# Kernel tuning notes

Hardware: AMD Instinct MI355X
Metric: run time of the kernel (lower is better)

Reference implementation:

```python
import jax, jax.numpy as jnp
import numpy as np

B, L, CIN, H, K = 32, 4096, 128, 256, 3


def setup_inputs() -> dict:
    key = jax.random.key(0)
    k1, k2, k3 = jax.random.split(key, 3)
    x = jax.random.normal(k1, (B, L, CIN), dtype=jnp.float32)
    # Conv1d weight: (out_ch=3H, in_ch=CIN, kernel=K), fan-in scaled like torch default
    W = jax.random.normal(k2, (3 * H, CIN, K), dtype=jnp.float32) * (1.0 / np.sqrt(CIN * K))
    b = jax.random.normal(k3, (3 * H,), dtype=jnp.float32) * 0.01
    return {"x": x, "W": W, "b": b}


def reference(x, W, b):
    # x: (B, L, CIN) -> (B, CIN, L), matching torch's x.transpose(1, 2)
    xc = jnp.transpose(x, (0, 2, 1))
    # valid 1D conv -> (B, 3H, T) with T = L - K + 1
    conv = jax.lax.conv_general_dilated(
        xc, W, window_strides=(1,), padding="VALID",
        dimension_numbers=("NCH", "OIH", "NCH"),
    ) + b[None, :, None]
    Z, F, O = jnp.split(conv, 3, axis=1)
    Z = jnp.tanh(Z)
    F = jax.nn.sigmoid(F)
    O = jax.nn.sigmoid(O)
    # sequential fo-pool: h_t = O_t * (F_t * h_{t-1} + (1 - F_t) * Z_t)
    zs = jnp.moveaxis(Z, 2, 0)   # (T, B, H)
    fs = jnp.moveaxis(F, 2, 0)
    os_ = jnp.moveaxis(O, 2, 0)
    h0 = jnp.zeros((x.shape[0], H), dtype=Z.dtype)

    def step(h, zfo):
        z, f, o = zfo
        h = o * (f * h + (1.0 - f) * z)
        return h, None

    hT, _ = jax.lax.scan(step, h0, (zs, fs, os_))
    return hT  # (B, H): final hidden state
```

## Files before the change

### kernel.cpp

```cpp
#include <hip/hip_runtime.h>
#include <math.h>

#define B_    32
#define L_    4096
#define CIN_  128
#define H_    256
#define T_    4094
#define KTOT_ 384

#define MT_   64
#define NTB_  64
#define NKT_  12

typedef float f32x4 __attribute__((ext_vector_type(4)));
typedef short s16x8 __attribute__((ext_vector_type(8)));

static __device__ __forceinline__ unsigned short f2bf(float f) {
  unsigned u = __builtin_bit_cast(unsigned, f);
  u = (u + 0x7FFFu + ((u >> 16) & 1u)) >> 16;
  return (unsigned short)u;
}

__global__ __launch_bounds__(256) void packW_bf16(const float* __restrict__ W,
                                                  unsigned short* __restrict__ Wb) {
  const int idx = blockIdx.x * 256 + threadIdx.x;
  const int c = idx % 768;
  const int t = idx / 768;
  const int kgrp = t & 3;
  const int kt = t >> 2;
  const int q = c >> 4, lr = c & 15;
  const int gate = q % 3, hgrp = q / 3;
  const int oc = gate * 256 + hgrp * 16 + lr;
  s16x8 outv;
#pragma unroll
  for (int e = 0; e < 8; ++e) {
    const int kk = kt * 32 + kgrp * 8 + e;
    const int i = kk & 127, k = kk >> 7;
    outv[e] = (short)f2bf(W[(size_t)oc * KTOT_ + i * 3 + k]);
  }
  *(s16x8*)(Wb + (size_t)idx * 8) = outv;
}

__global__ __launch_bounds__(1024, 4) void conv_scan_mfma(
    const float* __restrict__ x, const unsigned short* __restrict__ Wb,
    const float* __restrict__ bias, float* __restrict__ Pc,
    float* __restrict__ Sc) {
  __shared__ __align__(16) char xs[66 * 256];

  const int tid = threadIdx.x;
  const int wn = tid >> 6;
  const int l = tid & 63;
  const int lr = l & 15;
  const int lg = l >> 4;
  const int bid = blockIdx.x;
  const int bb = bid & 31;
  const int tblk = bid >> 5;
  const int t0 = tblk * MT_;

  const unsigned short* bp = Wb + lg * 6144 + (wn * 48 + lr) * 8;

  s16x8 bcur[3];
#pragma unroll
  for (int nj = 0; nj < 3; ++nj)
    bcur[nj] = *(const s16x8*)(bp + nj * 128);

  for (int v = tid; v < 66 * 32; v += 1024) {
    const int row = v >> 5;
    const int colb = (v & 31) * 8;
    int r = t0 + row;
    if (r > L_ - 1) r = L_ - 1;
    const float4 xv = *(const float4*)&x[((size_t)bb * L_ + r) * CIN_ + (v & 31) * 4];
    unsigned p0, p1;
    asm("v_cvt_pk_bf16_f32 %0, %1, %2" : "=v"(p0) : "v"(xv.x), "v"(xv.y));
    asm("v_cvt_pk_bf16_f32 %0, %1, %2" : "=v"(p1) : "v"(xv.z), "v"(xv.w));
    *(uint2*)(xs + row * 256 + (colb ^ ((row & 7) << 4))) = make_uint2(p0, p1);
  }

  f32x4 acc[4][3];
#pragma unroll
  for (int mi = 0; mi < 4; ++mi)
#pragma unroll
    for (int nj = 0; nj < 3; ++nj) acc[mi][nj] = (f32x4)0.f;

  __syncthreads();

#pragma unroll
  for (int kt = 0; kt < NKT_; ++kt) {
    s16x8 bnxt[3];
    if (kt < NKT_ - 1) {
#pragma unroll
      for (int nj = 0; nj < 3; ++nj)
        bnxt[nj] = *(const s16x8*)(bp + (kt + 1) * 24576 + nj * 128);
    }
    const int kof = kt >> 2;
    const int cb = (kt & 3) * 64 + lg * 16;
    s16x8 a[4];
#pragma unroll
    for (int mi = 0; mi < 4; ++mi) {
      const int row = mi * 16 + lr + kof;
      a[mi] = *(const s16x8*)(xs + row * 256 + (cb ^ ((row & 7) << 4)));
    }
#pragma unroll
    for (int mi = 0; mi < 4; ++mi)
#pragma unroll
      for (int nj = 0; nj < 3; ++nj)
        acc[mi][nj] = __builtin_amdgcn_mfma_f32_16x16x32_bf16(a[mi], bcur[nj], acc[mi][nj], 0, 0, 0);
    if (kt < NKT_ - 1) {
#pragma unroll
      for (int nj = 0; nj < 3; ++nj) bcur[nj] = bnxt[nj];
    }
  }

  const int hl = wn * 16 + lr;
  const float bz = bias[hl];
  const float bf_ = bias[256 + hl];
  const float bo_ = bias[512 + hl];

  float Pw = 1.f, Sw = 0.f;
#pragma unroll
  for (int mi = 0; mi < 4; ++mi) {
    float Pr = 1.f, Sr = 0.f;
#pragma unroll
    for (int r = 0; r < 4; ++r) {
      const int t = t0 + mi * 16 + lg * 4 + r;
      const float zr = acc[mi][0][r] + bz;
      const float fr = acc[mi][1][r] + bf_;
      const float orr = acc[mi][2][r] + bo_;
      const float zc = fminf(fmaxf(zr, -15.f), 15.f);
      const float e2 = __expf(2.f * zc);
      const float zt = (e2 - 1.f) * __builtin_amdgcn_rcpf(e2 + 1.f);
      const float ft = __builtin_amdgcn_rcpf(1.f + __expf(-fr));
      const float ot = __builtin_amdgcn_rcpf(1.f + __expf(-orr));
      float A = ot * ft;
      float Bv = ot * (1.f - ft) * zt;
      const bool valid = (t < T_);
      A = valid ? A : 1.f;
      Bv = valid ? Bv : 0.f;
      Sr = A * Sr + Bv;
      Pr = A * Pr;
    }
    float Pp = __shfl_xor(Pr, 16), Sp = __shfl_xor(Sr, 16);
    if (lg & 1) { Sr = Pr * Sp + Sr; Pr = Pr * Pp; }
    else        { Sr = Pp * Sr + Sp; Pr = Pp * Pr; }
    Pp = __shfl_xor(Pr, 32); Sp = __shfl_xor(Sr, 32);
    if (lg & 2) { Sr = Pr * Sp + Sr; Pr = Pr * Pp; }
    else        { Sr = Pp * Sr + Sp; Pr = Pp * Pr; }
    Sw = Pr * Sw + Sr;
    Pw = Pr * Pw;
  }

  if (lg == 0) {
    const size_t o = ((size_t)bb * NTB_ + tblk) * H_ + hl;
    Pc[o] = Pw;
    Sc[o] = Sw;
  }
}

__global__ __launch_bounds__(128) void combine_kernel(const float* __restrict__ Pc,
                                                      const float* __restrict__ Sc,
                                                      float* __restrict__ out) {
  const int idx = blockIdx.x * 128 + threadIdx.x;
  const int b = idx >> 8;
  const int h = idx & 255;
  float hv = 0.f;
#pragma unroll 8
  for (int c = 0; c < NTB_; ++c) {
    const float p = Pc[((size_t)b * NTB_ + c) * H_ + h];
    const float s = Sc[((size_t)b * NTB_ + c) * H_ + h];
    hv = p * hv + s;
  }
  out[idx] = hv;
}

extern "C" void kernel_launch(void* const* d_in, const int* in_sizes, int n_in,
                              void* d_out, int out_size, void* d_ws, size_t ws_size,
                              hipStream_t stream) {
  const float* x = (const float*)d_in[0];
  const float* W = (const float*)d_in[1];
  const float* bias = (const float*)d_in[2];
  float* out = (float*)d_out;

  char* ws = (char*)d_ws;
  unsigned short* Wb = (unsigned short*)ws;
  float* Pc = (float*)(ws + (1 << 20));
  float* Sc = (float*)(ws + 3 * (1 << 20));

  packW_bf16<<<144, 256, 0, stream>>>(W, Wb);
  conv_scan_mfma<<<2048, 1024, 0, stream>>>(x, Wb, bias, Pc, Sc);
  combine_kernel<<<64, 128, 0, stream>>>(Pc, Sc, out);
}
```

Measured before the change: 182.9 us.

## Make conv blocks persistent over four time tiles with double-buffered x prefetch

Each block now handles four time tiles (stride 16 tiles) instead of one, so the grid drops from 2048 to 512 blocks. The next tile's x rows are loaded into registers during the current tile's MFMA and scan work, then converted to bf16 and written into a second LDS buffer. The weight fragments stay in a register pipeline across tiles instead of being reloaded per block. The aim is to hide global load latency and cut per-block launch and startup cost, at the price of doubled LDS use, more registers for the prefetch, and fewer blocks to balance across CUs.

```diff
diff --git a/kernel.cpp b/kernel.cpp
--- a/kernel.cpp
+++ b/kernel.cpp
@@ -11,6 +11,7 @@
 #define MT_   64
 #define NTB_  64
 #define NKT_  12
+#define TPB_  4
 
 typedef float f32x4 __attribute__((ext_vector_type(4)));
 typedef short s16x8 __attribute__((ext_vector_type(8)));
@@ -45,17 +46,18 @@
     const float* __restrict__ x, const unsigned short* __restrict__ Wb,
     const float* __restrict__ bias, float* __restrict__ Pc,
     float* __restrict__ Sc) {
-  __shared__ __align__(16) char xs[66 * 256];
+  __shared__ __align__(16) char smem[2 * 66 * 256];
 
   const int tid = threadIdx.x;
   const int wn = tid >> 6;
   const int l = tid & 63;
   const int lr = l & 15;
   const int lg = l >> 4;
-  const int bid = blockIdx.x;
-  const int bb = bid & 31;
-  const int tblk = bid >> 5;
-  const int t0 = tblk * MT_;
+  const int p = blockIdx.x;
+  const int bb = p & 31;
+  const int tblk0 = p >> 5;
+
+  const float* xb = x + (size_t)bb * L_ * CIN_;
 
   const unsigned short* bp = Wb + lg * 6144 + (wn * 48 + lr) * 8;
 
@@ -63,96 +65,135 @@
 #pragma unroll
   for (int nj = 0; nj < 3; ++nj)
     bcur[nj] = *(const s16x8*)(bp + nj * 128);
-
-  for (int v = tid; v < 66 * 32; v += 1024) {
-    const int row = v >> 5;
-    const int colb = (v & 31) * 8;
-    int r = t0 + row;
-    if (r > L_ - 1) r = L_ - 1;
-    const float4 xv = *(const float4*)&x[((size_t)bb * L_ + r) * CIN_ + (v & 31) * 4];
-    unsigned p0, p1;
-    asm("v_cvt_pk_bf16_f32 %0, %1, %2" : "=v"(p0) : "v"(xv.x), "v"(xv.y));
-    asm("v_cvt_pk_bf16_f32 %0, %1, %2" : "=v"(p1) : "v"(xv.z), "v"(xv.w));
-    *(uint2*)(xs + row * 256 + (colb ^ ((row & 7) << 4))) = make_uint2(p0, p1);
-  }
-
-  f32x4 acc[4][3];
-#pragma unroll
-  for (int mi = 0; mi < 4; ++mi)
-#pragma unroll
-    for (int nj = 0; nj < 3; ++nj) acc[mi][nj] = (f32x4)0.f;
-
-  __syncthreads();
-
-#pragma unroll
-  for (int kt = 0; kt < NKT_; ++kt) {
-    s16x8 bnxt[3];
-    if (kt < NKT_ - 1) {
-#pragma unroll
-      for (int nj = 0; nj < 3; ++nj)
-        bnxt[nj] = *(const s16x8*)(bp + (kt + 1) * 24576 + nj * 128);
-    }
-    const int kof = kt >> 2;
-    const int cb = (kt & 3) * 64 + lg * 16;
-    s16x8 a[4];
-#pragma unroll
-    for (int mi = 0; mi < 4; ++mi) {
-      const int row = mi * 16 + lr + kof;
-      a[mi] = *(const s16x8*)(xs + row * 256 + (cb ^ ((row & 7) << 4)));
-    }
-#pragma unroll
-    for (int mi = 0; mi < 4; ++mi)
-#pragma unroll
-      for (int nj = 0; nj < 3; ++nj)
-        acc[mi][nj] = __builtin_amdgcn_mfma_f32_16x16x32_bf16(a[mi], bcur[nj], acc[mi][nj], 0, 0, 0);
-    if (kt < NKT_ - 1) {
-#pragma unroll
-      for (int nj = 0; nj < 3; ++nj) bcur[nj] = bnxt[nj];
-    }
-  }
 
   const int hl = wn * 16 + lr;
   const float bz = bias[hl];
   const float bf_ = bias[256 + hl];
   const float bo_ = bias[512 + hl];
 
-  float Pw = 1.f, Sw = 0.f;
-#pragma unroll
-  for (int mi = 0; mi < 4; ++mi) {
-    float Pr = 1.f, Sr = 0.f;
-#pragma unroll
-    for (int r = 0; r < 4; ++r) {
-      const int t = t0 + mi * 16 + lg * 4 + r;
-      const float zr = acc[mi][0][r] + bz;
-      const float fr = acc[mi][1][r] + bf_;
-      const float orr = acc[mi][2][r] + bo_;
-      const float zc = fminf(fmaxf(zr, -15.f), 15.f);
-      const float e2 = __expf(2.f * zc);
-      const float zt = (e2 - 1.f) * __builtin_amdgcn_rcpf(e2 + 1.f);
-      const float ft = __builtin_amdgcn_rcpf(1.f + __expf(-fr));
-      const float ot = __builtin_amdgcn_rcpf(1.f + __expf(-orr));
-      float A = ot * ft;
-      float Bv = ot * (1.f - ft) * zt;
-      const bool valid = (t < T_);
-      A = valid ? A : 1.f;
-      Bv = valid ? Bv : 0.f;
-      Sr = A * Sr + Bv;
-      Pr = A * Pr;
-    }
-    float Pp = __shfl_xor(Pr, 16), Sp = __shfl_xor(Sr, 16);
-    if (lg & 1) { Sr = Pr * Sp + Sr; Pr = Pr * Pp; }
-    else        { Sr = Pp * Sr + Sp; Pr = Pp * Pr; }
-    Pp = __shfl_xor(Pr, 32); Sp = __shfl_xor(Sr, 32);
-    if (lg & 2) { Sr = Pr * Sp + Sr; Pr = Pr * Pp; }
-    else        { Sr = Pp * Sr + Sp; Pr = Pp * Pr; }
-    Sw = Pr * Sw + Sr;
-    Pw = Pr * Pw;
-  }
-
-  if (lg == 0) {
-    const size_t o = ((size_t)bb * NTB_ + tblk) * H_ + hl;
-    Pc[o] = Pw;
-    Sc[o] = Sw;
+  char* cur = smem;
+  char* nxt = smem + 66 * 256;
+  {
+    const int t0 = tblk0 * MT_;
+#pragma unroll
+    for (int s = 0; s < 3; ++s) {
+      const int v = tid + 1024 * s;
+      if (v < 66 * 32) {
+        const int row = v >> 5;
+        int r = t0 + row;
+        if (r > L_ - 1) r = L_ - 1;
+        const float4 xv = *(const float4*)&xb[(size_t)r * CIN_ + (v & 31) * 4];
+        unsigned p0, p1;
+        asm("v_cvt_pk_bf16_f32 %0, %1, %2" : "=v"(p0) : "v"(xv.x), "v"(xv.y));
+        asm("v_cvt_pk_bf16_f32 %0, %1, %2" : "=v"(p1) : "v"(xv.z), "v"(xv.w));
+        *(uint2*)(cur + row * 256 + (((v & 31) * 8) ^ ((row & 7) << 4))) = make_uint2(p0, p1);
+      }
+    }
+  }
+  __syncthreads();
+
+  for (int j = 0; j < TPB_; ++j) {
+    const int tblk = tblk0 + 16 * j;
+    const int t0 = tblk * MT_;
+    const bool hn = (j + 1 < TPB_);
+
+    float4 xr[3];
+    if (hn) {
+      const int t0n = (tblk + 16) * MT_;
+#pragma unroll
+      for (int s = 0; s < 3; ++s) {
+        const int v = tid + 1024 * s;
+        if (v < 66 * 32) {
+          int r = t0n + (v >> 5);
+          if (r > L_ - 1) r = L_ - 1;
+          xr[s] = *(const float4*)&xb[(size_t)r * CIN_ + (v & 31) * 4];
+        }
+      }
+    }
+
+    f32x4 acc[4][3];
+#pragma unroll
+    for (int mi = 0; mi < 4; ++mi)
+#pragma unroll
+      for (int nj = 0; nj < 3; ++nj) acc[mi][nj] = (f32x4)0.f;
+
+#pragma unroll
+    for (int kt = 0; kt < NKT_; ++kt) {
+      s16x8 bnxt[3];
+      const int ktn = (kt + 1) % NKT_;
+#pragma unroll
+      for (int nj = 0; nj < 3; ++nj)
+        bnxt[nj] = *(const s16x8*)(bp + ktn * 24576 + nj * 128);
+      const int kof = kt >> 2;
+      const int cb = (kt & 3) * 64 + lg * 16;
+      s16x8 a[4];
+#pragma unroll
+      for (int mi = 0; mi < 4; ++mi) {
+        const int row = mi * 16 + lr + kof;
+        a[mi] = *(const s16x8*)(cur + row * 256 + (cb ^ ((row & 7) << 4)));
+      }
+#pragma unroll
+      for (int mi = 0; mi < 4; ++mi)
+#pragma unroll
+        for (int nj = 0; nj < 3; ++nj)
+          acc[mi][nj] = __builtin_amdgcn_mfma_f32_16x16x32_bf16(a[mi], bcur[nj], acc[mi][nj], 0, 0, 0);
+#pragma unroll
+      for (int nj = 0; nj < 3; ++nj) bcur[nj] = bnxt[nj];
+    }
+
+    float Pw = 1.f, Sw = 0.f;
+#pragma unroll
+    for (int mi = 0; mi < 4; ++mi) {
+      float Pr = 1.f, Sr = 0.f;
+#pragma unroll
+      for (int r = 0; r < 4; ++r) {
+        const int t = t0 + mi * 16 + lg * 4 + r;
+        const float zr = acc[mi][0][r] + bz;
+        const float fr = acc[mi][1][r] + bf_;
+        const float orr = acc[mi][2][r] + bo_;
+        const float zc = fminf(fmaxf(zr, -15.f), 15.f);
+        const float e2 = __expf(2.f * zc);
+        const float zt = (e2 - 1.f) * __builtin_amdgcn_rcpf(e2 + 1.f);
+        const float ft = __builtin_amdgcn_rcpf(1.f + __expf(-fr));
+        const float ot = __builtin_amdgcn_rcpf(1.f + __expf(-orr));
+        float A = ot * ft;
+        float Bv = ot * (1.f - ft) * zt;
+        const bool valid = (t < T_);
+        A = valid ? A : 1.f;
+        Bv = valid ? Bv : 0.f;
+        Sr = A * Sr + Bv;
+        Pr = A * Pr;
+      }
+      float Pp = __shfl_xor(Pr, 16), Sp = __shfl_xor(Sr, 16);
+      if (lg & 1) { Sr = Pr * Sp + Sr; Pr = Pr * Pp; }
+      else        { Sr = Pp * Sr + Sp; Pr = Pp * Pr; }
+      Pp = __shfl_xor(Pr, 32); Sp = __shfl_xor(Sr, 32);
+      if (lg & 2) { Sr = Pr * Sp + Sr; Pr = Pr * Pp; }
+      else        { Sr = Pp * Sr + Sp; Pr = Pp * Pr; }
+      Sw = Pr * Sw + Sr;
+      Pw = Pr * Pw;
+    }
+    if (lg == 0) {
+      const size_t o = ((size_t)bb * NTB_ + tblk) * H_ + hl;
+      Pc[o] = Pw;
+      Sc[o] = Sw;
+    }
+
+    if (hn) {
+#pragma unroll
+      for (int s = 0; s < 3; ++s) {
+        const int v = tid + 1024 * s;
+        if (v < 66 * 32) {
+          const int row = v >> 5;
+          unsigned p0, p1;
+          asm("v_cvt_pk_bf16_f32 %0, %1, %2" : "=v"(p0) : "v"(xr[s].x), "v"(xr[s].y));
+          asm("v_cvt_pk_bf16_f32 %0, %1, %2" : "=v"(p1) : "v"(xr[s].z), "v"(xr[s].w));
+          *(uint2*)(nxt + row * 256 + (((v & 31) * 8) ^ ((row & 7) << 4))) = make_uint2(p0, p1);
+        }
+      }
+    }
+    __syncthreads();
+    char* tmp = cur; cur = nxt; nxt = tmp;
   }
 }
 
@@ -186,6 +227,6 @@
   float* Sc = (float*)(ws + 3 * (1 << 20));
 
   packW_bf16<<<144, 256, 0, stream>>>(W, Wb);
-  conv_scan_mfma<<<2048, 1024, 0, stream>>>(x, Wb, bias, Pc, Sc);
+  conv_scan_mfma<<<512, 1024, 0, stream>>>(x, Wb, bias, Pc, Sc);
   combine_kernel<<<64, 128, 0, stream>>>(Pc, Sc, out);
 }
```

Measured after the change: 402.7 us. +120.2%, slower.
